# Optimization experiments

Measured on AMD Instinct MI355X. Metric: run time of the kernel, lower is better.

Reference implementation:

```python
import jax, jax.numpy as jnp
import numpy as np

N, L, C, H = 8, 2048, 512, 512
C_HALF = max(C // 2, 1)


def setup_inputs() -> dict:
    key = jax.random.key(0)
    ks = jax.random.split(key, 11)
    s = 0.02
    return {
        "x": jax.random.normal(ks[0], (N, L, C), dtype=jnp.float32),
        "theta_w": jax.random.normal(ks[1], (C, H), dtype=jnp.float32) * s,
        "theta_b": jax.random.normal(ks[2], (H,), dtype=jnp.float32) * s,
        "phi_w": jax.random.normal(ks[3], (C, H), dtype=jnp.float32) * s,
        "phi_b": jax.random.normal(ks[4], (H,), dtype=jnp.float32) * s,
        "psi_w": jax.random.normal(ks[5], (C, H), dtype=jnp.float32) * s,
        "psi_b": jax.random.normal(ks[6], (H,), dtype=jnp.float32) * s,
        "r1_w": jax.random.normal(ks[7], (H, C_HALF), dtype=jnp.float32) * s,
        "r1_b": jax.random.normal(ks[8], (C_HALF,), dtype=jnp.float32) * s,
        "r2_w": jax.random.normal(ks[9], (C_HALF, C), dtype=jnp.float32) * s,
        "r2_b": jax.random.normal(ks[10], (C,), dtype=jnp.float32) * s,
    }


def reference(x, theta_w, theta_b, phi_w, phi_b, psi_w, psi_b, r1_w, r1_b, r2_w, r2_b):
    # projections: [n, L, h]
    x_t = x @ theta_w + theta_b
    x_ph = x @ phi_w + phi_b
    x_psi = x @ psi_w + psi_b
    # unscaled attention: phi @ theta^T -> [n, L, L], softmax over last dim
    attn = jax.nn.softmax(jnp.einsum("nlh,nmh->nlm", x_ph, x_t), axis=2)
    x_add = jnp.einsum("nlm,nmh->nlh", attn, x_psi)
    # recover MLP with LeakyReLU(0.2) then Tanh, residual add
    h1 = jax.nn.leaky_relu(x_add @ r1_w + r1_b, negative_slope=0.2)
    h2 = jnp.tanh(h1 @ r2_w + r2_b)
    return x + h2
```

## Files before the change

### kernel.cpp

```cpp
#include <hip/hip_runtime.h>
#include <hip/hip_bf16.h>

typedef float f32x4 __attribute__((ext_vector_type(4)));
typedef int   v8i   __attribute__((ext_vector_type(8)));
typedef __attribute__((address_space(3))) unsigned int       lds_uint;
typedef __attribute__((address_space(1))) const unsigned int glb_uint;

__device__ __forceinline__ float tanh_fast(float x) {
    float e = __expf(-2.0f * fabsf(x));
    float r = (1.0f - e) / (1.0f + e);
    return copysignf(r, x);
}
__device__ __forceinline__ unsigned char f2fp8(float v) {
    return (unsigned char)(__builtin_amdgcn_cvt_pk_fp8_f32(v, 0.0f, 0, false) & 0xff);
}

__global__ __launch_bounds__(256) void prep(
    const float* __restrict__ x,
    const float* __restrict__ theta_w, const float* __restrict__ phi_w,
    const float* __restrict__ psi_w,   const float* __restrict__ r1_w,
    const float* __restrict__ r2_w,
    const float* __restrict__ theta_b, const float* __restrict__ phi_b,
    const float* __restrict__ psi_b,
    unsigned char* __restrict__ xb8, unsigned char* __restrict__ wCat8T,
    unsigned char* __restrict__ r1T8, unsigned char* __restrict__ r2T8,
    float* __restrict__ bCat) {
    const int b = blockIdx.x, t = threadIdx.x;
    if (b < 8192) {
        long i = ((long)b * 256 + t) * 4;
        float4 f = *(const float4*)(x + i);
        int w = __builtin_amdgcn_cvt_pk_fp8_f32(f.x, f.y, 0, false);
        w = __builtin_amdgcn_cvt_pk_fp8_f32(f.z, f.w, w, true);
        *(unsigned int*)(xb8 + i) = (unsigned int)w;
    } else if (b < 11264) {
        const int sel = (b - 8192) >> 10;
        const int idx = ((b - 8192) & 1023) * 256 + t;
        const float* w = sel == 0 ? theta_w : (sel == 1 ? phi_w : psi_w);
        const int r = idx >> 9, c = idx & 511;
        wCat8T[(long)(sel * 512 + c) * 512 + r] = f2fp8(w[idx] * 16.0f);
    } else if (b < 11776) {
        const int idx = (b - 11264) * 256 + t;
        const int r = idx >> 8, c = idx & 255;
        r1T8[(long)c * 512 + r] = f2fp8(r1_w[idx] * 16.0f);
    } else if (b < 12288) {
        const int idx = (b - 11776) * 256 + t;
        const int r = idx >> 9, c = idx & 511;
        r2T8[(long)c * 256 + r] = f2fp8(r2_w[idx] * 16.0f);
    } else {
        const int i = (b - 12288) * 256 + t;
        if (i < 1536)
            bCat[i] = i < 512 ? theta_b[i] : (i < 1024 ? phi_b[i - 512] : psi_b[i - 1024]);
    }
}

template <int MODE>
__global__ __launch_bounds__(256) void gemm_fp8(
    const unsigned char* __restrict__ A,
    const unsigned char* __restrict__ Bt,
    const float* __restrict__ bias,
    const float* __restrict__ resid,
    unsigned char* __restrict__ out8,
    unsigned char* __restrict__ out8b,
    unsigned char* __restrict__ outV,
    float* __restrict__ outF,
    int K, int ldaB, int ldbB, int ldc, long sA, long sB, long sC) {
    __shared__ unsigned char As[2][128 * 128];
    __shared__ unsigned char Bs[2][128 * 128];

    const int tid  = threadIdx.x;
    const int lane = tid & 63, wave = tid >> 6;
    const int m16  = lane & 15, quad = lane >> 4;
    const int wm   = (wave >> 1) << 6, wn = (wave & 1) << 6;
    const int m0   = blockIdx.x << 7, n0 = blockIdx.y << 7;

    const int srow = lane >> 3;
    const int uswz = (lane & 7) ^ srow;

    const unsigned char* Abase = A  + (long)blockIdx.z * sA + (long)m0 * ldaB;
    const unsigned char* Bbase = Bt + (long)blockIdx.z * sB + (long)n0 * ldbB;
    const int stR = (wave << 5) + srow;
    const long gA0 = (long)stR * ldaB + (uswz << 4);
    const long gB0 = (long)stR * ldbB + (uswz << 4);

    const int s8  = m16 & 7;
    const int P   = quad ^ (s8 >> 1);
    const int cLo = (P << 1) + (s8 & 1);
    const int offLo = cLo << 4;
    const int offHi = (cLo ^ 1) << 4;

    f32x4 acc[4][4] = {};
    union F8 { v8i v; int4 q[2]; };

    auto STAGE = [&](int buf, int kk) {
#pragma unroll
        for (int i = 0; i < 4; ++i) {
            const unsigned char* gp = Abase + gA0 + (long)(i << 3) * ldaB + kk;
            unsigned char* lp = &As[buf][((wave << 5) + (i << 3)) << 7];
            __builtin_amdgcn_global_load_lds((glb_uint*)gp, (lds_uint*)lp, 16, 0, 0);
        }
#pragma unroll
        for (int i = 0; i < 4; ++i) {
            const unsigned char* gp = Bbase + gB0 + (long)(i << 3) * ldbB + kk;
            unsigned char* lp = &Bs[buf][((wave << 5) + (i << 3)) << 7];
            __builtin_amdgcn_global_load_lds((glb_uint*)gp, (lds_uint*)lp, 16, 0, 0);
        }
    };

    STAGE(0, 0);
    int cur = 0;
    for (int k0 = 0; k0 < K; k0 += 128) {
        if (k0 + 128 < K) {
            STAGE(cur ^ 1, k0 + 128);
            asm volatile("s_waitcnt vmcnt(8)" ::: "memory");
        } else {
            asm volatile("s_waitcnt vmcnt(0)" ::: "memory");
        }
        asm volatile("s_barrier" ::: "memory");

        const unsigned char* Ab = As[cur];
        const unsigned char* Bb = Bs[cur];
        F8 af[4], bg[4];
#pragma unroll
        for (int f = 0; f < 4; ++f) {
            const int m = wm + (f << 4) + m16;
            const int n = wn + (f << 4) + m16;
            af[f].q[0] = *(const int4*)&Ab[(m << 7) + offLo];
            af[f].q[1] = *(const int4*)&Ab[(m << 7) + offHi];
            bg[f].q[0] = *(const int4*)&Bb[(n << 7) + offLo];
            bg[f].q[1] = *(const int4*)&Bb[(n << 7) + offHi];
        }
#pragma unroll
        for (int fi = 0; fi < 4; ++fi)
#pragma unroll
            for (int fj = 0; fj < 4; ++fj)
                acc[fi][fj] = __builtin_amdgcn_mfma_scale_f32_16x16x128_f8f6f4(
                    af[fi].v, bg[fj].v, acc[fi][fj],
                    0, 0, 0, 127, 0, 127);

        asm volatile("s_waitcnt lgkmcnt(0)" ::: "memory");
        asm volatile("s_barrier" ::: "memory");
        cur ^= 1;
    }

    if (MODE == 0) {
        const int sel = n0 >> 9;
        if (sel < 2) {
            unsigned char* dst = sel == 0 ? out8 : out8b;
#pragma unroll
            for (int fj = 0; fj < 4; ++fj) {
                const int col = n0 + wn + (fj << 4) + m16;
                const int cb  = col & 511;
                const float bv = bias[col];
#pragma unroll
                for (int fi = 0; fi < 4; ++fi)
#pragma unroll
                    for (int r = 0; r < 4; ++r) {
                        const int row = m0 + wm + (fi << 4) + (quad << 2) + r;
                        dst[(long)row * 512 + cb] = f2fp8(acc[fi][fj][r] * 0.0625f + bv);
                    }
            }
        } else {
            const int z = m0 >> 11, l0 = (m0 & 2047) + wm + (quad << 2);
#pragma unroll
            for (int fj = 0; fj < 4; ++fj) {
                const int col = n0 + wn + (fj << 4) + m16;
                const int h   = col & 511;
                const float bv = bias[col];
#pragma unroll
                for (int fi = 0; fi < 4; ++fi) {
                    int w = __builtin_amdgcn_cvt_pk_fp8_f32(
                        acc[fi][fj][0] * 0.0625f + bv, acc[fi][fj][1] * 0.0625f + bv, 0, false);
                    w = __builtin_amdgcn_cvt_pk_fp8_f32(
                        acc[fi][fj][2] * 0.0625f + bv, acc[fi][fj][3] * 0.0625f + bv, w, true);
                    *(unsigned int*)(outV + ((long)z * 512 + h) * 2048 + l0 + (fi << 4)) =
                        (unsigned int)w;
                }
            }
        }
    } else {
#pragma unroll
        for (int fj = 0; fj < 4; ++fj) {
            const int col = n0 + wn + (fj << 4) + m16;
            const float bv = bias[col];
#pragma unroll
            for (int fi = 0; fi < 4; ++fi)
#pragma unroll
                for (int r = 0; r < 4; ++r) {
                    const int row = m0 + wm + (fi << 4) + (quad << 2) + r;
                    float v = acc[fi][fj][r] * 0.0625f + bv;
                    if (MODE == 3) {
                        v = v > 0.0f ? v : 0.2f * v;
                        out8[(long)row * 256 + col] = f2fp8(v);
                    } else {
                        const long idx = (long)row * ldc + col;
                        outF[idx] = tanh_fast(v) + resid[idx];
                    }
                }
        }
    }
}

__global__ __launch_bounds__(512) void flash(
    const unsigned char* __restrict__ Qg8,
    const unsigned char* __restrict__ Kg8,
    const unsigned char* __restrict__ Vg8,
    unsigned char* __restrict__ out8) {
    __shared__ unsigned char Qs[64 * 512];
    __shared__ unsigned char Ks[2][128 * 128];
    __shared__ unsigned char Vs[512 * 128];
    __shared__ unsigned char Ps[64 * 128];
    __shared__ float smax[2][32][4];
    __shared__ float ssum[2][32][4];

    const int tid  = threadIdx.x;
    const int lane = tid & 63, wave = tid >> 6;
    const int m16  = lane & 15, quad = lane >> 4;
    const int lg   = wave >> 2;
    const int mw   = wave & 3;
    const int z    = blockIdx.y;
    const int l0   = blockIdx.x << 6;

    const unsigned char* Qg = Qg8 + ((long)z * 2048 + l0) * 512;
    const unsigned char* Kg = Kg8 + (long)z * 2048 * 512;
    const unsigned char* Vg = Vg8 + (long)z * 512 * 2048;

    const int s8  = m16 & 7;
    const int cLo = ((quad ^ (s8 >> 1)) << 1) + (s8 & 1);
    const int offLo = cLo << 4, offHi = (cLo ^ 1) << 4;

    auto stageQ = [&]() {
#pragma unroll
        for (int i = 0; i < 4; ++i) {
            const int slot = wave * 4 + i;
            const int row  = slot * 2 + (lane >> 5);
            const int w5   = lane & 31;
            const int su   = (w5 & 24) | ((w5 & 7) ^ (row & 7));
            const unsigned char* gp = Qg + (long)row * 512 + (su << 4);
            __builtin_amdgcn_global_load_lds((glb_uint*)gp, (lds_uint*)&Qs[slot << 10], 16, 0, 0);
        }
    };
    auto stageK = [&](int t) {
        const int c = t >> 2, ks = t & 3;
#pragma unroll
        for (int i = 0; i < 2; ++i) {
            const int slot = wave * 2 + i;
            const int row  = (slot << 3) + (lane >> 3);
            const int su   = (lane & 7) ^ (row & 7);
            const unsigned char* gp = Kg + (long)(c * 128 + row) * 512 + ks * 128 + (su << 4);
            __builtin_amdgcn_global_load_lds((glb_uint*)gp, (lds_uint*)&Ks[t & 1][slot << 10], 16, 0, 0);
        }
    };
    auto stageV = [&](int c) {
#pragma unroll
        for (int i = 0; i < 8; ++i) {
            const int slot = wave * 8 + i;
            const int row  = (slot << 3) + (lane >> 3);
            const int su   = (lane & 7) ^ (row & 7);
            const unsigned char* gp = Vg + (long)row * 2048 + c * 128 + (su << 4);
            __builtin_amdgcn_global_load_lds((glb_uint*)gp, (lds_uint*)&Vs[slot << 10], 16, 0, 0);
        }
    };

    f32x4 U[2][8] = {};
    float m_run[2][4], l_run[2][4];
#pragma unroll
    for (int a = 0; a < 2; ++a)
#pragma unroll
        for (int b = 0; b < 4; ++b) { m_run[a][b] = -3.0e38f; l_run[a][b] = 0.0f; }

    union F8 { v8i v; int4 q[2]; };

    stageQ();
    stageK(0);

    for (int c = 0; c < 16; ++c) {
        f32x4 sacc[2][2] = {};
#pragma unroll
        for (int ks = 0; ks < 4; ++ks) {
            const int t = c * 4 + ks;
            if (t + 1 < 64) stageK(t + 1);
            if (ks == 1) stageV(c);
            if (ks == 0) {
                asm volatile("s_waitcnt vmcnt(2)" ::: "memory");
            } else if (ks == 3) {
                if (c == 15) asm volatile("s_waitcnt vmcnt(0)" ::: "memory");
                else         asm volatile("s_waitcnt vmcnt(2)" ::: "memory");
            } else {
                asm volatile("s_waitcnt vmcnt(10)" ::: "memory");
            }
            asm volatile("s_barrier" ::: "memory");

            const unsigned char* Kb = Ks[t & 1];
            F8 aq[2], bk[2];
#pragma unroll
            for (int f = 0; f < 2; ++f) {
                const int l = lg * 32 + f * 16 + m16;
                aq[f].q[0] = *(const int4*)&Qs[l * 512 + ks * 128 + offLo];
                aq[f].q[1] = *(const int4*)&Qs[l * 512 + ks * 128 + offHi];
                const int m = mw * 32 + f * 16 + m16;
                bk[f].q[0] = *(const int4*)&Kb[(m << 7) + offLo];
                bk[f].q[1] = *(const int4*)&Kb[(m << 7) + offHi];
            }
#pragma unroll
            for (int fi = 0; fi < 2; ++fi)
#pragma unroll
                for (int fj = 0; fj < 2; ++fj)
                    sacc[fi][fj] = __builtin_amdgcn_mfma_scale_f32_16x16x128_f8f6f4(
                        aq[fi].v, bk[fj].v, sacc[fi][fj], 0, 0, 0, 127, 0, 127);

            asm volatile("s_waitcnt lgkmcnt(0)" ::: "memory");
            asm volatile("s_barrier" ::: "memory");
        }

        float pm[2][4];
#pragma unroll
        for (int fi = 0; fi < 2; ++fi)
#pragma unroll
            for (int r = 0; r < 4; ++r) {
                float v = fmaxf(sacc[fi][0][r], sacc[fi][1][r]);
#pragma unroll
                for (int off = 1; off < 16; off <<= 1) v = fmaxf(v, __shfl_xor(v, off));
                pm[fi][r] = v;
            }
        if (m16 == 0) {
#pragma unroll
            for (int fi = 0; fi < 2; ++fi)
#pragma unroll
                for (int r = 0; r < 4; ++r)
                    smax[lg][fi * 16 + quad * 4 + r][mw] = pm[fi][r];
        }
        asm volatile("s_waitcnt lgkmcnt(0)" ::: "memory");
        asm volatile("s_barrier" ::: "memory");

        float alpha[2][4], p[2][2][4];
#pragma unroll
        for (int fi = 0; fi < 2; ++fi)
#pragma unroll
            for (int r = 0; r < 4; ++r) {
                const int rr = fi * 16 + quad * 4 + r;
                float cm = fmaxf(fmaxf(smax[lg][rr][0], smax[lg][rr][1]),
                                 fmaxf(smax[lg][rr][2], smax[lg][rr][3]));
                const float mo = m_run[fi][r];
                const float mn = fmaxf(mo, cm);
                m_run[fi][r] = mn;
                alpha[fi][r] = __expf(mo - mn);
#pragma unroll
                for (int fj = 0; fj < 2; ++fj)
                    p[fi][fj][r] = __expf(sacc[fi][fj][r] - mn);
            }
#pragma unroll
        for (int fi = 0; fi < 2; ++fi)
#pragma unroll
            for (int fh = 0; fh < 8; ++fh)
#pragma unroll
                for (int r = 0; r < 4; ++r)
                    U[fi][fh][r] *= alpha[fi][r];
        float ps[2][4];
#pragma unroll
        for (int fi = 0; fi < 2; ++fi)
#pragma unroll
            for (int r = 0; r < 4; ++r) {
                float v = p[fi][0][r] + p[fi][1][r];
#pragma unroll
                for (int off = 1; off < 16; off <<= 1) v += __shfl_xor(v, off);
                ps[fi][r] = v;
            }
        if (m16 == 0) {
#pragma unroll
            for (int fi = 0; fi < 2; ++fi)
#pragma unroll
                for (int r = 0; r < 4; ++r)
                    ssum[lg][fi * 16 + quad * 4 + r][mw] = ps[fi][r];
        }
#pragma unroll
        for (int fi = 0; fi < 2; ++fi)
#pragma unroll
            for (int r = 0; r < 4; ++r) {
                const int l = lg * 32 + fi * 16 + quad * 4 + r;
#pragma unroll
                for (int fj = 0; fj < 2; ++fj) {
                    const int m = mw * 32 + fj * 16 + m16;
                    Ps[(l << 7) + ((((m >> 4) ^ (l & 7)) << 4) | (m & 15))] =
                        f2fp8(p[fi][fj][r] * 256.0f);
                }
            }
        asm volatile("s_waitcnt vmcnt(2) lgkmcnt(0)" ::: "memory");
        asm volatile("s_barrier" ::: "memory");

#pragma unroll
        for (int fi = 0; fi < 2; ++fi)
#pragma unroll
            for (int r = 0; r < 4; ++r) {
                const int rr = fi * 16 + quad * 4 + r;
                l_run[fi][r] = l_run[fi][r] * alpha[fi][r] +
                               ssum[lg][rr][0] + ssum[lg][rr][1] +
                               ssum[lg][rr][2] + ssum[lg][rr][3];
            }

        F8 pa[2];
#pragma unroll
        for (int f = 0; f < 2; ++f) {
            const int l = lg * 32 + f * 16 + m16;
            pa[f].q[0] = *(const int4*)&Ps[(l << 7) + offLo];
            pa[f].q[1] = *(const int4*)&Ps[(l << 7) + offHi];
        }
#pragma unroll
        for (int fh = 0; fh < 8; ++fh) {
            F8 vb;
            const int h = mw * 128 + fh * 16 + m16;
            vb.q[0] = *(const int4*)&Vs[(h << 7) + offLo];
            vb.q[1] = *(const int4*)&Vs[(h << 7) + offHi];
#pragma unroll
            for (int fi = 0; fi < 2; ++fi)
                U[fi][fh] = __builtin_amdgcn_mfma_scale_f32_16x16x128_f8f6f4(
                    pa[fi].v, vb.v, U[fi][fh], 0, 0, 0, 127, 0, 127);
        }
        asm volatile("s_waitcnt lgkmcnt(0)" ::: "memory");
        asm volatile("s_barrier" ::: "memory");
    }

#pragma unroll
    for (int fi = 0; fi < 2; ++fi)
#pragma unroll
        for (int r = 0; r < 4; ++r) {
            const float inv = 1.0f / (256.0f * l_run[fi][r]);
            const long row = (long)z * 2048 + l0 + lg * 32 + fi * 16 + quad * 4 + r;
#pragma unroll
            for (int fh = 0; fh < 8; ++fh) {
                const int h = mw * 128 + fh * 16 + m16;
                out8[row * 512 + h] = f2fp8(U[fi][fh][r] * inv);
            }
        }
}

extern "C" void kernel_launch(void* const* d_in, const int* in_sizes, int n_in,
                              void* d_out, int out_size, void* d_ws, size_t ws_size,
                              hipStream_t stream) {
    const float* x       = (const float*)d_in[0];
    const float* theta_w = (const float*)d_in[1];
    const float* theta_b = (const float*)d_in[2];
    const float* phi_w   = (const float*)d_in[3];
    const float* phi_b   = (const float*)d_in[4];
    const float* psi_w   = (const float*)d_in[5];
    const float* psi_b   = (const float*)d_in[6];
    const float* r1_w    = (const float*)d_in[7];
    const float* r1_b    = (const float*)d_in[8];
    const float* r2_w    = (const float*)d_in[9];
    const float* r2_b    = (const float*)d_in[10];
    float* out = (float*)d_out;

    constexpr int  N = 8, L = 2048, C = 512, H = 512, CH = 256;
    constexpr long NL = (long)N * L;

    char* p = (char*)d_ws;
    auto alloc = [&](size_t bytes) { void* q = (void*)p; p += bytes; return q; };
    unsigned char*  xb8    = (unsigned char*)alloc(NL * C);
    unsigned char*  TH8    = (unsigned char*)alloc(NL * H);
    unsigned char*  PH8    = (unsigned char*)alloc(NL * H);
    unsigned char*  VT8    = (unsigned char*)alloc((long)N * H * L);
    unsigned char*  xadd8  = (unsigned char*)alloc(NL * H);
    unsigned char*  h18    = (unsigned char*)alloc(NL * CH);
    unsigned char*  wCat8T = (unsigned char*)alloc((long)1536 * 512);
    unsigned char*  r1T8   = (unsigned char*)alloc((long)H * CH);
    unsigned char*  r2T8   = (unsigned char*)alloc((long)CH * C);
    float*          bCat   = (float*)alloc(1536 * 4 + 256);

    prep<<<12294, 256, 0, stream>>>(x, theta_w, phi_w, psi_w, r1_w, r2_w,
                                    theta_b, phi_b, psi_b, xb8, wCat8T, r1T8, r2T8, bCat);

    gemm_fp8<0><<<dim3(NL / 128, 1536 / 128, 1), 256, 0, stream>>>(
        xb8, wCat8T, bCat, nullptr, TH8, PH8, VT8, nullptr,
        C, C, C, 0, 0, 0, 0);

    flash<<<dim3(L / 64, N, 1), 512, 0, stream>>>(PH8, TH8, VT8, xadd8);

    gemm_fp8<3><<<dim3(NL / 128, CH / 128, 1), 256, 0, stream>>>(
        xadd8, r1T8, r1_b, nullptr, h18, nullptr, nullptr, nullptr,
        H, H, H, CH, 0, 0, 0);

    gemm_fp8<4><<<dim3(NL / 128, C / 128, 1), 256, 0, stream>>>(
        h18, r2T8, r2_b, x, nullptr, nullptr, nullptr, out,
        CH, CH, CH, C, 0, 0, 0);
}
```

Measured before the change: 257.9 us.

## Keep Q in registers, stage full K chunk per block, request two blocks per CU

Q fragments now load straight from global memory into registers once, so the Q shared-memory buffer and its per-step reads go away. K for a whole 128-key chunk (all four k-slices) is staged at once into a four-slot buffer, and prefetch of the next K and V chunk is issued after the barriers that free them. This drops the per-k-step trailing barrier and changes the vmcnt wait schedule. Launch bounds now ask for two 512-thread blocks per CU, which caps registers while Q sits in them, so spills are possible.

New measurement: 392.6 us. 1.52x slower.

```diff
diff --git a/kernel.cpp b/kernel.cpp
--- a/kernel.cpp
+++ b/kernel.cpp
@@ -200,13 +200,12 @@
     }
 }
 
-__global__ __launch_bounds__(512) void flash(
+__global__ __launch_bounds__(512, 2) void flash(
     const unsigned char* __restrict__ Qg8,
     const unsigned char* __restrict__ Kg8,
     const unsigned char* __restrict__ Vg8,
     unsigned char* __restrict__ out8) {
-    __shared__ unsigned char Qs[64 * 512];
-    __shared__ unsigned char Ks[2][128 * 128];
+    __shared__ unsigned char Ks[4][128 * 128];
     __shared__ unsigned char Vs[512 * 128];
     __shared__ unsigned char Ps[64 * 128];
     __shared__ float smax[2][32][4];
@@ -228,33 +227,36 @@
     const int cLo = ((quad ^ (s8 >> 1)) << 1) + (s8 & 1);
     const int offLo = cLo << 4, offHi = (cLo ^ 1) << 4;
 
-    auto stageQ = [&]() {
-#pragma unroll
-        for (int i = 0; i < 4; ++i) {
-            const int slot = wave * 4 + i;
-            const int row  = slot * 2 + (lane >> 5);
-            const int w5   = lane & 31;
-            const int su   = (w5 & 24) | ((w5 & 7) ^ (row & 7));
-            const unsigned char* gp = Qg + (long)row * 512 + (su << 4);
-            __builtin_amdgcn_global_load_lds((glb_uint*)gp, (lds_uint*)&Qs[slot << 10], 16, 0, 0);
-        }
-    };
-    auto stageK = [&](int t) {
-        const int c = t >> 2, ks = t & 3;
-#pragma unroll
-        for (int i = 0; i < 2; ++i) {
-            const int slot = wave * 2 + i;
-            const int row  = (slot << 3) + (lane >> 3);
+    union F8 { v8i v; int4 q[2]; };
+
+    F8 qf[2][4];
+#pragma unroll
+    for (int fi = 0; fi < 2; ++fi)
+#pragma unroll
+        for (int ks = 0; ks < 4; ++ks) {
+            const int l = lg * 32 + fi * 16 + m16;
+            qf[fi][ks].q[0] = *(const int4*)(Qg + (long)l * 512 + ks * 128 + quad * 32);
+            qf[fi][ks].q[1] = *(const int4*)(Qg + (long)l * 512 + ks * 128 + quad * 32 + 16);
+        }
+    asm volatile("" ::: "memory");
+
+    auto stageK = [&](int c) {
+#pragma unroll
+        for (int i = 0; i < 8; ++i) {
+            const int slot = i * 8 + wave;
+            const int t    = slot >> 4;
+            const int seg  = slot & 15;
+            const int row  = seg * 8 + (lane >> 3);
             const int su   = (lane & 7) ^ (row & 7);
-            const unsigned char* gp = Kg + (long)(c * 128 + row) * 512 + ks * 128 + (su << 4);
-            __builtin_amdgcn_global_load_lds((glb_uint*)gp, (lds_uint*)&Ks[t & 1][slot << 10], 16, 0, 0);
+            const unsigned char* gp = Kg + (long)(c * 128 + row) * 512 + t * 128 + (su << 4);
+            __builtin_amdgcn_global_load_lds((glb_uint*)gp, (lds_uint*)&Ks[t][seg << 10], 16, 0, 0);
         }
     };
     auto stageV = [&](int c) {
 #pragma unroll
         for (int i = 0; i < 8; ++i) {
-            const int slot = wave * 8 + i;
-            const int row  = (slot << 3) + (lane >> 3);
+            const int slot = i * 8 + wave;
+            const int row  = slot * 8 + (lane >> 3);
             const int su   = (lane & 7) ^ (row & 7);
             const unsigned char* gp = Vg + (long)row * 2048 + c * 128 + (su << 4);
             __builtin_amdgcn_global_load_lds((glb_uint*)gp, (lds_uint*)&Vs[slot << 10], 16, 0, 0);
@@ -268,48 +270,32 @@
 #pragma unroll
         for (int b = 0; b < 4; ++b) { m_run[a][b] = -3.0e38f; l_run[a][b] = 0.0f; }
 
-    union F8 { v8i v; int4 q[2]; };
-
-    stageQ();
     stageK(0);
+    stageV(0);
 
     for (int c = 0; c < 16; ++c) {
         f32x4 sacc[2][2] = {};
 #pragma unroll
         for (int ks = 0; ks < 4; ++ks) {
-            const int t = c * 4 + ks;
-            if (t + 1 < 64) stageK(t + 1);
-            if (ks == 1) stageV(c);
-            if (ks == 0) {
-                asm volatile("s_waitcnt vmcnt(2)" ::: "memory");
-            } else if (ks == 3) {
-                if (c == 15) asm volatile("s_waitcnt vmcnt(0)" ::: "memory");
-                else         asm volatile("s_waitcnt vmcnt(2)" ::: "memory");
-            } else {
-                asm volatile("s_waitcnt vmcnt(10)" ::: "memory");
-            }
-            asm volatile("s_barrier" ::: "memory");
-
-            const unsigned char* Kb = Ks[t & 1];
-            F8 aq[2], bk[2];
+            if (ks == 0)      asm volatile("s_waitcnt vmcnt(14)" ::: "memory");
+            else if (ks == 1) asm volatile("s_waitcnt vmcnt(12)" ::: "memory");
+            else if (ks == 2) asm volatile("s_waitcnt vmcnt(10)" ::: "memory");
+            else              asm volatile("s_waitcnt vmcnt(8)"  ::: "memory");
+            __builtin_amdgcn_s_barrier();
+
+            F8 bk[2];
 #pragma unroll
             for (int f = 0; f < 2; ++f) {
-                const int l = lg * 32 + f * 16 + m16;
-                aq[f].q[0] = *(const int4*)&Qs[l * 512 + ks * 128 + offLo];
-                aq[f].q[1] = *(const int4*)&Qs[l * 512 + ks * 128 + offHi];
                 const int m = mw * 32 + f * 16 + m16;
-                bk[f].q[0] = *(const int4*)&Kb[(m << 7) + offLo];
-                bk[f].q[1] = *(const int4*)&Kb[(m << 7) + offHi];
+                bk[f].q[0] = *(const int4*)&Ks[ks][(m << 7) + offLo];
+                bk[f].q[1] = *(const int4*)&Ks[ks][(m << 7) + offHi];
             }
 #pragma unroll
             for (int fi = 0; fi < 2; ++fi)
 #pragma unroll
                 for (int fj = 0; fj < 2; ++fj)
                     sacc[fi][fj] = __builtin_amdgcn_mfma_scale_f32_16x16x128_f8f6f4(
-                        aq[fi].v, bk[fj].v, sacc[fi][fj], 0, 0, 0, 127, 0, 127);
-
-            asm volatile("s_waitcnt lgkmcnt(0)" ::: "memory");
-            asm volatile("s_barrier" ::: "memory");
+                        qf[fi][ks].v, bk[fj].v, sacc[fi][fj], 0, 0, 0, 127, 0, 127);
         }
 
         float pm[2][4];
@@ -330,7 +316,8 @@
                     smax[lg][fi * 16 + quad * 4 + r][mw] = pm[fi][r];
         }
         asm volatile("s_waitcnt lgkmcnt(0)" ::: "memory");
-        asm volatile("s_barrier" ::: "memory");
+        __builtin_amdgcn_s_barrier();
+        if (c + 1 < 16) stageK(c + 1);
 
         float alpha[2][4], p[2][2][4];
 #pragma unroll
@@ -384,8 +371,10 @@
                         f2fp8(p[fi][fj][r] * 256.0f);
                 }
             }
-        asm volatile("s_waitcnt vmcnt(2) lgkmcnt(0)" ::: "memory");
-        asm volatile("s_barrier" ::: "memory");
+        if (c < 15) asm volatile("s_waitcnt vmcnt(8)" ::: "memory");
+        else        asm volatile("s_waitcnt vmcnt(0)" ::: "memory");
+        asm volatile("s_waitcnt lgkmcnt(0)" ::: "memory");
+        __builtin_amdgcn_s_barrier();
 
 #pragma unroll
         for (int fi = 0; fi < 2; ++fi)
@@ -416,7 +405,8 @@
                     pa[fi].v, vb.v, U[fi][fh], 0, 0, 0, 127, 0, 127);
         }
         asm volatile("s_waitcnt lgkmcnt(0)" ::: "memory");
-        asm volatile("s_barrier" ::: "memory");
+        __builtin_amdgcn_s_barrier();
+        if (c + 1 < 16) stageV(c + 1);
     }
 
 #pragma unroll
```

## Restructure flash kernel to 32-row query tiles with streamed double-buffered V

Applied to the files above, without the earlier changes.

The flash attention kernel now handles 32 query rows per block instead of 64, which doubles the grid. Each of the 8 waves owns one 16-key column slice, and V is streamed in 128-row chunks through two ping-pong LDS buffers instead of being staged whole. LDS is packed into one aliased buffer, launch bounds request more occupancy, MFMA sections are given higher priority, and the accumulator rescale is skipped when no row maximum grows. In exchange, K/V traffic per query row doubles and there are more barriers per chunk, while per-block LDS and register footprint shrink.

Measured after the change: 584.8 us. +126.7%, slower.

```diff
diff --git a/kernel.cpp b/kernel.cpp
--- a/kernel.cpp
+++ b/kernel.cpp
@@ -200,191 +200,191 @@
     }
 }
 
-__global__ __launch_bounds__(512) void flash(
+__global__ __launch_bounds__(512, 4) void flash(
     const unsigned char* __restrict__ Qg8,
     const unsigned char* __restrict__ Kg8,
     const unsigned char* __restrict__ Vg8,
     unsigned char* __restrict__ out8) {
-    __shared__ unsigned char Qs[64 * 512];
-    __shared__ unsigned char Ks[2][128 * 128];
-    __shared__ unsigned char Vs[512 * 128];
-    __shared__ unsigned char Ps[64 * 128];
-    __shared__ float smax[2][32][4];
-    __shared__ float ssum[2][32][4];
+    __shared__ unsigned char lds[81920];
+    unsigned char* Qs  = lds;
+    unsigned char* Ks0 = lds + 16384;
+    unsigned char* Ks1 = lds + 32768;
+    unsigned char* Vs0 = lds + 49152;
+    unsigned char* Vs1 = lds + 65536;
+    unsigned char* Ps  = Ks1;
+    float* sx = (float*)(Ks1 + 4096);
+    float* sy = (float*)(Ks1 + 5120);
 
     const int tid  = threadIdx.x;
     const int lane = tid & 63, wave = tid >> 6;
     const int m16  = lane & 15, quad = lane >> 4;
-    const int lg   = wave >> 2;
-    const int mw   = wave & 3;
     const int z    = blockIdx.y;
-    const int l0   = blockIdx.x << 6;
+    const int l0   = blockIdx.x << 5;
 
     const unsigned char* Qg = Qg8 + ((long)z * 2048 + l0) * 512;
     const unsigned char* Kg = Kg8 + (long)z * 2048 * 512;
     const unsigned char* Vg = Vg8 + (long)z * 512 * 2048;
 
     const int s8  = m16 & 7;
-    const int cLo = ((quad ^ (s8 >> 1)) << 1) + (s8 & 1);
-    const int offLo = cLo << 4, offHi = (cLo ^ 1) << 4;
+    const int cL  = ((quad ^ (s8 >> 1)) << 1) + (s8 & 1);
+    const int offLo = cL << 4, offHi = (cL ^ 1) << 4;
+
+    union F8 { v8i v; int4 q[2]; };
 
     auto stageQ = [&]() {
-#pragma unroll
-        for (int i = 0; i < 4; ++i) {
-            const int slot = wave * 4 + i;
-            const int row  = slot * 2 + (lane >> 5);
-            const int w5   = lane & 31;
-            const int su   = (w5 & 24) | ((w5 & 7) ^ (row & 7));
-            const unsigned char* gp = Qg + (long)row * 512 + (su << 4);
-            __builtin_amdgcn_global_load_lds((glb_uint*)gp, (lds_uint*)&Qs[slot << 10], 16, 0, 0);
-        }
-    };
-    auto stageK = [&](int t) {
-        const int c = t >> 2, ks = t & 3;
 #pragma unroll
         for (int i = 0; i < 2; ++i) {
             const int slot = wave * 2 + i;
-            const int row  = (slot << 3) + (lane >> 3);
-            const int su   = (lane & 7) ^ (row & 7);
-            const unsigned char* gp = Kg + (long)(c * 128 + row) * 512 + ks * 128 + (su << 4);
-            __builtin_amdgcn_global_load_lds((glb_uint*)gp, (lds_uint*)&Ks[t & 1][slot << 10], 16, 0, 0);
+            const int row  = slot * 2 + (lane >> 5);
+            const int u    = lane & 31;
+            const int su   = (u & 24) | ((u & 7) ^ (row & 7));
+            __builtin_amdgcn_global_load_lds(
+                (glb_uint*)(Qg + (long)row * 512 + (su << 4)),
+                (lds_uint*)(Qs + (slot << 10)), 16, 0, 0);
         }
     };
-    auto stageV = [&](int c) {
-#pragma unroll
-        for (int i = 0; i < 8; ++i) {
-            const int slot = wave * 8 + i;
-            const int row  = (slot << 3) + (lane >> 3);
-            const int su   = (lane & 7) ^ (row & 7);
-            const unsigned char* gp = Vg + (long)row * 2048 + c * 128 + (su << 4);
-            __builtin_amdgcn_global_load_lds((glb_uint*)gp, (lds_uint*)&Vs[slot << 10], 16, 0, 0);
+    auto stageK = [&](int c, int t) {
+        unsigned char* base = (t & 1) ? Ks1 : Ks0;
+#pragma unroll
+        for (int i = 0; i < 2; ++i) {
+            const int slot = wave * 2 + i;
+            const int r    = (slot << 3) + (lane >> 3);
+            const int su   = (lane & 7) ^ (r & 7);
+            __builtin_amdgcn_global_load_lds(
+                (glb_uint*)(Kg + (long)(c * 128 + r) * 512 + t * 128 + (su << 4)),
+                (lds_uint*)(base + (slot << 10)), 16, 0, 0);
         }
     };
-
-    f32x4 U[2][8] = {};
-    float m_run[2][4], l_run[2][4];
+    auto stageV = [&](int c, int j) {
+        unsigned char* base = (j & 1) ? Vs1 : Vs0;
+#pragma unroll
+        for (int i = 0; i < 2; ++i) {
+            const int slot = wave * 2 + i;
+            const int r    = (slot << 3) + (lane >> 3);
+            const int su   = (lane & 7) ^ (r & 7);
+            __builtin_amdgcn_global_load_lds(
+                (glb_uint*)(Vg + (long)(j * 128 + r) * 2048 + c * 128 + (su << 4)),
+                (lds_uint*)(base + (slot << 10)), 16, 0, 0);
+        }
+    };
+
+    f32x4 U[2][4] = {};
+    float m_run[2][4], l_run[2][4], alpha[2][4];
 #pragma unroll
     for (int a = 0; a < 2; ++a)
 #pragma unroll
         for (int b = 0; b < 4; ++b) { m_run[a][b] = -3.0e38f; l_run[a][b] = 0.0f; }
 
-    union F8 { v8i v; int4 q[2]; };
-
     stageQ();
-    stageK(0);
+    stageK(0, 0);
 
     for (int c = 0; c < 16; ++c) {
-        f32x4 sacc[2][2] = {};
+        f32x4 sacc[2] = {};
 #pragma unroll
         for (int ks = 0; ks < 4; ++ks) {
-            const int t = c * 4 + ks;
-            if (t + 1 < 64) stageK(t + 1);
-            if (ks == 1) stageV(c);
-            if (ks == 0) {
-                asm volatile("s_waitcnt vmcnt(2)" ::: "memory");
-            } else if (ks == 3) {
-                if (c == 15) asm volatile("s_waitcnt vmcnt(0)" ::: "memory");
-                else         asm volatile("s_waitcnt vmcnt(2)" ::: "memory");
-            } else {
-                asm volatile("s_waitcnt vmcnt(10)" ::: "memory");
-            }
+            if (ks == 0) { if (c == 0) asm volatile("s_waitcnt vmcnt(0)" ::: "memory"); }
+            else if (ks == 1) asm volatile("s_waitcnt vmcnt(2)" ::: "memory");
+            else              asm volatile("s_waitcnt vmcnt(0)" ::: "memory");
             asm volatile("s_barrier" ::: "memory");
-
-            const unsigned char* Kb = Ks[t & 1];
-            F8 aq[2], bk[2];
-#pragma unroll
-            for (int f = 0; f < 2; ++f) {
-                const int l = lg * 32 + f * 16 + m16;
-                aq[f].q[0] = *(const int4*)&Qs[l * 512 + ks * 128 + offLo];
-                aq[f].q[1] = *(const int4*)&Qs[l * 512 + ks * 128 + offHi];
-                const int m = mw * 32 + f * 16 + m16;
-                bk[f].q[0] = *(const int4*)&Kb[(m << 7) + offLo];
-                bk[f].q[1] = *(const int4*)&Kb[(m << 7) + offHi];
-            }
-#pragma unroll
-            for (int fi = 0; fi < 2; ++fi)
-#pragma unroll
-                for (int fj = 0; fj < 2; ++fj)
-                    sacc[fi][fj] = __builtin_amdgcn_mfma_scale_f32_16x16x128_f8f6f4(
-                        aq[fi].v, bk[fj].v, sacc[fi][fj], 0, 0, 0, 127, 0, 127);
-
-            asm volatile("s_waitcnt lgkmcnt(0)" ::: "memory");
-            asm volatile("s_barrier" ::: "memory");
-        }
-
-        float pm[2][4];
+            if (ks == 0) { stageK(c, 1); stageV(c, 0); }
+            else if (ks == 1) stageK(c, 2);
+            else if (ks == 2) stageK(c, 3);
+            else { stageV(c, 1); if (c + 1 < 16) stageK(c + 1, 0); }
+
+            const unsigned char* Kb = (ks & 1) ? Ks1 : Ks0;
+            F8 aq[2], bk;
+#pragma unroll
+            for (int fi = 0; fi < 2; ++fi) {
+                const int l = fi * 16 + m16;
+                aq[fi].q[0] = *(const int4*)&Qs[l * 512 + ks * 128 + offLo];
+                aq[fi].q[1] = *(const int4*)&Qs[l * 512 + ks * 128 + offHi];
+            }
+            const int m = wave * 16 + m16;
+            bk.q[0] = *(const int4*)&Kb[(m << 7) + offLo];
+            bk.q[1] = *(const int4*)&Kb[(m << 7) + offHi];
+            __builtin_amdgcn_s_setprio(1);
+#pragma unroll
+            for (int fi = 0; fi < 2; ++fi)
+                sacc[fi] = __builtin_amdgcn_mfma_scale_f32_16x16x128_f8f6f4(
+                    aq[fi].v, bk.v, sacc[fi], 0, 0, 0, 127, 0, 127);
+            __builtin_amdgcn_s_setprio(0);
+        }
+        asm volatile("s_barrier" ::: "memory");
+
+        float cm[2][4];
 #pragma unroll
         for (int fi = 0; fi < 2; ++fi)
 #pragma unroll
             for (int r = 0; r < 4; ++r) {
-                float v = fmaxf(sacc[fi][0][r], sacc[fi][1][r]);
+                float v = sacc[fi][r];
 #pragma unroll
                 for (int off = 1; off < 16; off <<= 1) v = fmaxf(v, __shfl_xor(v, off));
-                pm[fi][r] = v;
+                cm[fi][r] = v;
             }
         if (m16 == 0) {
 #pragma unroll
             for (int fi = 0; fi < 2; ++fi)
 #pragma unroll
                 for (int r = 0; r < 4; ++r)
-                    smax[lg][fi * 16 + quad * 4 + r][mw] = pm[fi][r];
+                    sx[(fi * 16 + quad * 4 + r) * 8 + wave] = cm[fi][r];
         }
         asm volatile("s_waitcnt lgkmcnt(0)" ::: "memory");
         asm volatile("s_barrier" ::: "memory");
 
-        float alpha[2][4], p[2][2][4];
+        bool grow = false;
 #pragma unroll
         for (int fi = 0; fi < 2; ++fi)
 #pragma unroll
             for (int r = 0; r < 4; ++r) {
                 const int rr = fi * 16 + quad * 4 + r;
-                float cm = fmaxf(fmaxf(smax[lg][rr][0], smax[lg][rr][1]),
-                                 fmaxf(smax[lg][rr][2], smax[lg][rr][3]));
-                const float mo = m_run[fi][r];
-                const float mn = fmaxf(mo, cm);
-                m_run[fi][r] = mn;
-                alpha[fi][r] = __expf(mo - mn);
-#pragma unroll
-                for (int fj = 0; fj < 2; ++fj)
-                    p[fi][fj][r] = __expf(sacc[fi][fj][r] - mn);
-            }
+                float m1 = fmaxf(fmaxf(sx[rr * 8 + 0], sx[rr * 8 + 1]),
+                                 fmaxf(sx[rr * 8 + 2], sx[rr * 8 + 3]));
+                float m2 = fmaxf(fmaxf(sx[rr * 8 + 4], sx[rr * 8 + 5]),
+                                 fmaxf(sx[rr * 8 + 6], sx[rr * 8 + 7]));
+                cm[fi][r] = fmaxf(m1, m2);
+                grow |= (cm[fi][r] > m_run[fi][r]);
+            }
+        if (__ballot(grow)) {
+#pragma unroll
+            for (int fi = 0; fi < 2; ++fi)
+#pragma unroll
+                for (int r = 0; r < 4; ++r) {
+                    const float mn = fmaxf(m_run[fi][r], cm[fi][r]);
+                    alpha[fi][r] = __expf(m_run[fi][r] - mn);
+                    m_run[fi][r] = mn;
+                }
+#pragma unroll
+            for (int fi = 0; fi < 2; ++fi)
+#pragma unroll
+                for (int j = 0; j < 4; ++j)
+#pragma unroll
+                    for (int r = 0; r < 4; ++r)
+                        U[fi][j][r] *= alpha[fi][r];
+        } else {
+#pragma unroll
+            for (int fi = 0; fi < 2; ++fi)
+#pragma unroll
+                for (int r = 0; r < 4; ++r) alpha[fi][r] = 1.0f;
+        }
+        float p[2][4];
 #pragma unroll
         for (int fi = 0; fi < 2; ++fi)
 #pragma unroll
-            for (int fh = 0; fh < 8; ++fh)
-#pragma unroll
-                for (int r = 0; r < 4; ++r)
-                    U[fi][fh][r] *= alpha[fi][r];
-        float ps[2][4];
+            for (int r = 0; r < 4; ++r) {
+                p[fi][r] = __expf(sacc[fi][r] - m_run[fi][r]);
+                float v = p[fi][r];
+#pragma unroll
+                for (int off = 1; off < 16; off <<= 1) v += __shfl_xor(v, off);
+                if (m16 == 0) sy[(fi * 16 + quad * 4 + r) * 8 + wave] = v;
+            }
 #pragma unroll
         for (int fi = 0; fi < 2; ++fi)
 #pragma unroll
             for (int r = 0; r < 4; ++r) {
-                float v = p[fi][0][r] + p[fi][1][r];
-#pragma unroll
-                for (int off = 1; off < 16; off <<= 1) v += __shfl_xor(v, off);
-                ps[fi][r] = v;
-            }
-        if (m16 == 0) {
-#pragma unroll
-            for (int fi = 0; fi < 2; ++fi)
-#pragma unroll
-                for (int r = 0; r < 4; ++r)
-                    ssum[lg][fi * 16 + quad * 4 + r][mw] = ps[fi][r];
-        }
-#pragma unroll
-        for (int fi = 0; fi < 2; ++fi)
-#pragma unroll
-            for (int r = 0; r < 4; ++r) {
-                const int l = lg * 32 + fi * 16 + quad * 4 + r;
-#pragma unroll
-                for (int fj = 0; fj < 2; ++fj) {
-                    const int m = mw * 32 + fj * 16 + m16;
-                    Ps[(l << 7) + ((((m >> 4) ^ (l & 7)) << 4) | (m & 15))] =
-                        f2fp8(p[fi][fj][r] * 256.0f);
-                }
-            }
-        asm volatile("s_waitcnt vmcnt(2) lgkmcnt(0)" ::: "memory");
+                const int l = fi * 16 + quad * 4 + r;
+                Ps[(l << 7) + ((wave ^ (l & 7)) << 4) + m16] = f2fp8(p[fi][r] * 256.0f);
+            }
+        asm volatile("s_waitcnt lgkmcnt(0)" ::: "memory");
         asm volatile("s_barrier" ::: "memory");
 
 #pragma unroll
@@ -392,31 +392,71 @@
 #pragma unroll
             for (int r = 0; r < 4; ++r) {
                 const int rr = fi * 16 + quad * 4 + r;
-                l_run[fi][r] = l_run[fi][r] * alpha[fi][r] +
-                               ssum[lg][rr][0] + ssum[lg][rr][1] +
-                               ssum[lg][rr][2] + ssum[lg][rr][3];
-            }
-
+                float s = ((sy[rr * 8 + 0] + sy[rr * 8 + 1]) + (sy[rr * 8 + 2] + sy[rr * 8 + 3]))
+                        + ((sy[rr * 8 + 4] + sy[rr * 8 + 5]) + (sy[rr * 8 + 6] + sy[rr * 8 + 7]));
+                l_run[fi][r] = l_run[fi][r] * alpha[fi][r] + s;
+            }
         F8 pa[2];
 #pragma unroll
-        for (int f = 0; f < 2; ++f) {
-            const int l = lg * 32 + f * 16 + m16;
-            pa[f].q[0] = *(const int4*)&Ps[(l << 7) + offLo];
-            pa[f].q[1] = *(const int4*)&Ps[(l << 7) + offHi];
-        }
-#pragma unroll
-        for (int fh = 0; fh < 8; ++fh) {
+        for (int fi = 0; fi < 2; ++fi) {
+            const int l = fi * 16 + m16;
+            pa[fi].q[0] = *(const int4*)&Ps[(l << 7) + offLo];
+            pa[fi].q[1] = *(const int4*)&Ps[(l << 7) + offHi];
+        }
+        const int hl = wave * 16 + m16;
+        {
             F8 vb;
-            const int h = mw * 128 + fh * 16 + m16;
-            vb.q[0] = *(const int4*)&Vs[(h << 7) + offLo];
-            vb.q[1] = *(const int4*)&Vs[(h << 7) + offHi];
-#pragma unroll
-            for (int fi = 0; fi < 2; ++fi)
-                U[fi][fh] = __builtin_amdgcn_mfma_scale_f32_16x16x128_f8f6f4(
-                    pa[fi].v, vb.v, U[fi][fh], 0, 0, 0, 127, 0, 127);
-        }
-        asm volatile("s_waitcnt lgkmcnt(0)" ::: "memory");
-        asm volatile("s_barrier" ::: "memory");
+            vb.q[0] = *(const int4*)&Vs0[(hl << 7) + offLo];
+            vb.q[1] = *(const int4*)&Vs0[(hl << 7) + offHi];
+            __builtin_amdgcn_s_setprio(1);
+#pragma unroll
+            for (int fi = 0; fi < 2; ++fi)
+                U[fi][0] = __builtin_amdgcn_mfma_scale_f32_16x16x128_f8f6f4(
+                    pa[fi].v, vb.v, U[fi][0], 0, 0, 0, 127, 0, 127);
+            __builtin_amdgcn_s_setprio(0);
+        }
+        if (c + 1 < 16) asm volatile("s_waitcnt vmcnt(2)" ::: "memory");
+        else            asm volatile("s_waitcnt vmcnt(0)" ::: "memory");
+        asm volatile("s_barrier" ::: "memory");
+        stageV(c, 2);
+        {
+            F8 vb;
+            vb.q[0] = *(const int4*)&Vs1[(hl << 7) + offLo];
+            vb.q[1] = *(const int4*)&Vs1[(hl << 7) + offHi];
+            __builtin_amdgcn_s_setprio(1);
+#pragma unroll
+            for (int fi = 0; fi < 2; ++fi)
+                U[fi][1] = __builtin_amdgcn_mfma_scale_f32_16x16x128_f8f6f4(
+                    pa[fi].v, vb.v, U[fi][1], 0, 0, 0, 127, 0, 127);
+            __builtin_amdgcn_s_setprio(0);
+        }
+        asm volatile("s_waitcnt vmcnt(0)" ::: "memory");
+        asm volatile("s_barrier" ::: "memory");
+        stageV(c, 3);
+        {
+            F8 vb;
+            vb.q[0] = *(const int4*)&Vs0[(hl << 7) + offLo];
+            vb.q[1] = *(const int4*)&Vs0[(hl << 7) + offHi];
+            __builtin_amdgcn_s_setprio(1);
+#pragma unroll
+            for (int fi = 0; fi < 2; ++fi)
+                U[fi][2] = __builtin_amdgcn_mfma_scale_f32_16x16x128_f8f6f4(
+                    pa[fi].v, vb.v, U[fi][2], 0, 0, 0, 127, 0, 127);
+            __builtin_amdgcn_s_setprio(0);
+        }
+        asm volatile("s_waitcnt vmcnt(0)" ::: "memory");
+        asm volatile("s_barrier" ::: "memory");
+        {
+            F8 vb;
+            vb.q[0] = *(const int4*)&Vs1[(hl << 7) + offLo];
+            vb.q[1] = *(const int4*)&Vs1[(hl << 7) + offHi];
+            __builtin_amdgcn_s_setprio(1);
+#pragma unroll
+            for (int fi = 0; fi < 2; ++fi)
+                U[fi][3] = __builtin_amdgcn_mfma_scale_f32_16x16x128_f8f6f4(
+                    pa[fi].v, vb.v, U[fi][3], 0, 0, 0, 127, 0, 127);
+            __builtin_amdgcn_s_setprio(0);
+        }
     }
 
 #pragma unroll
@@ -424,11 +464,11 @@
 #pragma unroll
         for (int r = 0; r < 4; ++r) {
             const float inv = 1.0f / (256.0f * l_run[fi][r]);
-            const long row = (long)z * 2048 + l0 + lg * 32 + fi * 16 + quad * 4 + r;
-#pragma unroll
-            for (int fh = 0; fh < 8; ++fh) {
-                const int h = mw * 128 + fh * 16 + m16;
-                out8[row * 512 + h] = f2fp8(U[fi][fh][r] * inv);
+            const long row = (long)z * 2048 + l0 + fi * 16 + quad * 4 + r;
+#pragma unroll
+            for (int j = 0; j < 4; ++j) {
+                const int h = j * 128 + wave * 16 + m16;
+                out8[row * 512 + h] = f2fp8(U[fi][j][r] * inv);
             }
         }
 }
@@ -472,7 +512,7 @@
         xb8, wCat8T, bCat, nullptr, TH8, PH8, VT8, nullptr,
         C, C, C, 0, 0, 0, 0);
 
-    flash<<<dim3(L / 64, N, 1), 512, 0, stream>>>(PH8, TH8, VT8, xadd8);
+    flash<<<dim3(L / 32, N, 1), 512, 0, stream>>>(PH8, TH8, VT8, xadd8);
 
     gemm_fp8<3><<<dim3(NL / 128, CH / 128, 1), 256, 0, stream>>>(
         xadd8, r1T8, r1_b, nullptr, h18, nullptr, nullptr, nullptr,
```
